# Kernel tuning notes

Measured on AMD Instinct MI355X. Metric: run time of the kernel, lower is better.

Reference implementation:

```python
import jax, jax.numpy as jnp
import numpy as np

B, NV, FD = 16, 128, 8192
T_TEMP = 0.2      # self.T
MARGIN = 1.0      # nn.TripletMarginLoss default
EPS = 1e-6        # pairwise_distance eps


def _l2norm(x):
    # torch F.normalize(dim=1): x / max(||x||, 1e-12)
    nrm = jnp.maximum(jnp.linalg.norm(x, axis=-1, keepdims=True), 1e-12)
    return x / nrm


def _ssl_parts(qb, kb, nb, num_gt):
    # qb,kb,nb: [NV, FD] flattened reid embeddings for one image
    qv = _l2norm(qb)[:num_gt]          # [g, FD]
    kv = _l2norm(kb)[:num_gt]          # [g, FD]
    nv = _l2norm(nb)                   # [NV, FD] (negatives are NOT sliced)
    g = num_gt
    S = qv @ kv.T                      # [g, g] all pairwise dots (replaces torch.dot loops)
    # similarity-matrix loss
    sm = jnp.sum((S - jnp.eye(g, dtype=S.dtype)) ** 2) / (g * g)
    # pairwise distances with torch eps convention: ||a - b + eps||_2
    # = sqrt(||a||^2 + ||b||^2 - 2 a.b + 2*eps*(sum(a)-sum(b)) + D*eps^2); ||a||=||b||=1
    sq = qv.sum(axis=1)                # [g]
    sk = kv.sum(axis=1)                # [g]
    const = FD * EPS * EPS
    d_qk = jnp.sqrt(jnp.maximum(2.0 - 2.0 * S + 2.0 * EPS * (sq[:, None] - sk[None, :]) + const, 0.0))
    d_kq = jnp.sqrt(jnp.maximum(2.0 - 2.0 * S.T + 2.0 * EPS * (sk[:, None] - sq[None, :]) + const, 0.0))
    off = 1.0 - jnp.eye(g, dtype=S.dtype)
    # triplet: anc=q_i,pos=k_i,neg=k_j  and  anc=k_i,pos=q_i,neg=q_j, j != i
    tri1 = jnp.sum(jax.nn.relu(jnp.diag(d_qk)[:, None] - d_qk + MARGIN) * off)
    tri2 = jnp.sum(jax.nn.relu(jnp.diag(d_kq)[:, None] - d_kq + MARGIN) * off)
    tri_sum = tri1 + tri2
    # cycle consistency: |q_i.k_j - k_i.q_j| = |S[i,j] - S[j,i]|
    cyc = jnp.sum(jnp.abs(S - S.T) * off) / (g * (g - 1))
    # InfoNCE: l_pos = q_i.k_i, l_neg = q @ n.T
    l_pos = jnp.diag(S)[:, None]       # [g, 1]
    l_neg = qv @ nv.T                  # [g, NV]
    logits = jnp.concatenate([l_pos, l_neg], axis=1) / T_TEMP
    ce = jnp.mean(jax.nn.logsumexp(logits, axis=1) - logits[:, 0])  # CE with labels=0
    return sm, tri_sum, cyc, ce / g


def setup_inputs() -> dict:
    key = jax.random.key(0)
    kq, kk, kn = jax.random.split(key, 3)
    q = jax.random.normal(kq, (B, NV, FD), dtype=jnp.float32)
    k = jax.random.normal(kk, (B, NV, FD), dtype=jnp.float32)
    n = jax.random.normal(kn, (B, NV, FD), dtype=jnp.float32)
    return {"q": q, "k": k, "n": n, "num_gt": NV}


def reference(q, k, n, num_gt):
    sm, tri, cyc, ce = jax.vmap(lambda a, b, c: _ssl_parts(a, b, c, num_gt))(q, k, n)
    tri_cnt = 2 * num_gt * (num_gt - 1)
    # original bug: tri_loss accumulates across batches while tri_cnt resets,
    # so each batch contributes cumsum(tri)[b] / tri_cnt
    ssl = jnp.sum(sm) + jnp.sum(jnp.cumsum(tri)) / tri_cnt + jnp.sum(cyc) + jnp.sum(ce)
    return ssl
```

## Files before the change

### kernel.cpp

```cpp
#include <hip/hip_runtime.h>
#include <cstdint>
#include <cstddef>

#define B_N   16
#define G_N   128
#define FD_N  8192
#define KCH_N 8
#define KCB   1024
#define BKB   64
#define NST   16
#define NROWS 6144

typedef unsigned short u16;
typedef u16  u16x4 __attribute__((ext_vector_type(4)));
typedef u16  u16x8 __attribute__((ext_vector_type(8)));
typedef __bf16 bf16x8 __attribute__((ext_vector_type(8)));
typedef float f32x16 __attribute__((ext_vector_type(16)));

#define QSUM_P   0
#define QSSQ_P   32768
#define KSUM_P   65536
#define KSSQ_P   98304
#define NSSQ_P   131072
#define SM_ROW   163840
#define CE_ROW   165888
#define S_OFF    167936
#define PART_OFF_F 430080
#define BF16_OFF_F 2527232

__device__ __forceinline__ u16 f2bf(float f) {
    uint32_t u = __float_as_uint(f);
    u += 0x7FFFu + ((u >> 16) & 1u);
    return (u16)(u >> 16);
}

__device__ __forceinline__ void load_lds16(const float* g, float* l) {
    __builtin_amdgcn_global_load_lds(
        (__attribute__((address_space(1))) void*)(g),
        (__attribute__((address_space(3))) void*)(l),
        16, 0, 0);
}

#define WAITV4() asm volatile("s_waitcnt vmcnt(4)" ::: "memory")
#define WAITV0() asm volatile("s_waitcnt vmcnt(0)" ::: "memory")

__global__ __launch_bounds__(256)
void k_prep(const float* __restrict__ q, const float* __restrict__ kM,
            const float* __restrict__ nM, float* __restrict__ ws)
{
    const int lane = threadIdx.x & 63;
    const int wv   = threadIdx.x >> 6;
    const int R    = blockIdx.x * 4 + wv;
    const int mat  = R >> 11;
    const int r    = R & 2047;

    const float* src = (mat == 0 ? q : (mat == 1 ? kM : nM)) + (size_t)r * FD_N;
    u16* dst = (u16*)(ws + BF16_OFF_F) + (size_t)R * FD_N;

    float ss = 0.f, qq = 0.f;
    #pragma unroll 8
    for (int j = 0; j < 32; ++j) {
        const float4 v = *(const float4*)(src + (size_t)(j*64 + lane)*4);
        ss += (v.x + v.y) + (v.z + v.w);
        qq += v.x*v.x + v.y*v.y + v.z*v.z + v.w*v.w;
        u16x4 h;
        h[0]=f2bf(v.x); h[1]=f2bf(v.y); h[2]=f2bf(v.z); h[3]=f2bf(v.w);
        *(u16x4*)(dst + (size_t)(j*64 + lane)*4) = h;
    }
    #pragma unroll
    for (int m = 32; m >= 1; m >>= 1) {
        ss += __shfl_xor(ss, m, 64);
        qq += __shfl_xor(qq, m, 64);
    }
    if (lane == 0) {
        if (mat == 0)      { ws[QSUM_P + r] = ss; ws[QSSQ_P + r] = qq; }
        else if (mat == 1) { ws[KSUM_P + r] = ss; ws[KSSQ_P + r] = qq; }
        else               { ws[NSSQ_P + r] = qq; }
    }
}

__global__ __launch_bounds__(512, 2)
void k_mm(float* __restrict__ ws)
{
    __shared__ __align__(16) u16 sA[2][G_N * BKB];
    __shared__ __align__(16) u16 sB[2][G_N * BKB];

    const int tid = threadIdx.x;
    const int blk = blockIdx.x;
    const int b    = blk >> 4;
    const int rem  = blk & 15;
    const int half = rem >> 3;
    const int kch  = rem & 7;

    const int lane  = tid & 63;
    const int wv    = tid >> 6;
    const int wm    = wv >> 2;
    const int wn    = wv & 3;
    const int khalf = lane >> 5;
    const int lrow  = lane & 31;
    const int rA0 = wm*64 + lrow;
    const int rB0 = wn*32 + lrow;

    const u16* bf = (const u16*)(ws + BF16_OFF_F);
    const u16* Abase = bf + (size_t)(b*G_N) * FD_N + kch*KCB;
    const u16* Bbase = bf + (size_t)(((half ? 2 : 1)*2048) + b*G_N) * FD_N + kch*KCB;

    const int srow = wv*16 + (lane >> 3);
    const size_t gsw = (size_t)srow * FD_N + (size_t)(((lane & 7) ^ (srow & 7)) << 3);
    const int l0 = wv * 1024;
    const int l1 = l0 + 512;

#define STAGE(ST, T) do {                                                     \
        const size_t tof_ = gsw + (size_t)((T) * BKB);                        \
        load_lds16((const float*)(Abase + tof_),            (float*)(&sA[ST][l0])); \
        load_lds16((const float*)(Bbase + tof_),            (float*)(&sB[ST][l0])); \
        load_lds16((const float*)(Abase + tof_ + 8*FD_N),   (float*)(&sA[ST][l1])); \
        load_lds16((const float*)(Bbase + tof_ + 8*FD_N),   (float*)(&sB[ST][l1])); \
    } while (0)

#define FRAG(SP, R, KC)                                                       \
    __builtin_bit_cast(bf16x8, *(const u16x8*)((SP) + (R)*BKB +               \
        ((((KC)*2 + khalf) ^ ((R)&7)) << 3)))

#define COMPUTE(ST) do {                                                      \
        const u16* dA_ = &sA[ST][0];                                          \
        const u16* dB_ = &sB[ST][0];                                          \
        __builtin_amdgcn_s_setprio(1);                                        \
        _Pragma("unroll")                                                     \
        for (int kc = 0; kc < 4; ++kc) {                                      \
            bf16x8 a0_ = FRAG(dA_, rA0,      kc);                             \
            bf16x8 a1_ = FRAG(dA_, rA0 + 32, kc);                             \
            bf16x8 b0_ = FRAG(dB_, rB0,      kc);                             \
            acc[0] = __builtin_amdgcn_mfma_f32_32x32x16_bf16(a0_, b0_, acc[0], 0,0,0); \
            acc[1] = __builtin_amdgcn_mfma_f32_32x32x16_bf16(a1_, b0_, acc[1], 0,0,0); \
        }                                                                     \
        __builtin_amdgcn_s_setprio(0);                                        \
    } while (0)

    f32x16 acc[2];
    #pragma unroll
    for (int mb = 0; mb < 2; ++mb)
      #pragma unroll
      for (int e = 0; e < 16; ++e) acc[mb][e] = 0.f;

    STAGE(0, 0);
    STAGE(1, 1);

    for (int t = 0; t < NST - 2; t += 2) {
        WAITV4();
        __builtin_amdgcn_s_barrier();
        COMPUTE(0);
        __builtin_amdgcn_s_barrier();
        STAGE(0, t + 2);

        WAITV4();
        __builtin_amdgcn_s_barrier();
        COMPUTE(1);
        __builtin_amdgcn_s_barrier();
        STAGE(1, t + 3);
    }
    WAITV4();
    __builtin_amdgcn_s_barrier();
    COMPUTE(0);
    __builtin_amdgcn_s_barrier();
    WAITV0();
    __builtin_amdgcn_s_barrier();
    COMPUTE(1);

    u16* part = (u16*)(ws + PART_OFF_F) + ((size_t)blk << 14);
    #pragma unroll
    for (int mb = 0; mb < 2; ++mb) {
        const int col = wn*32 + lrow;
        const int rbase = wm*64 + mb*32 + 4*khalf;
        #pragma unroll
        for (int reg = 0; reg < 16; ++reg) {
            const int row = rbase + (reg & 3) + 8*(reg >> 2);
            part[row*G_N + col] = f2bf(acc[mb][reg]);
        }
    }
#undef STAGE
#undef FRAG
#undef COMPUTE
}

__global__ __launch_bounds__(256)
void k_red2(float* __restrict__ ws, float* __restrict__ out)
{
    const int blk  = blockIdx.x;
    const int b    = blk >> 4;
    const int half = (blk >> 3) & 1;
    const int rg   = blk & 7;
    const int t    = threadIdx.x;
    const int lr   = t >> 4;
    const int i    = rg*16 + lr;
    const int c8   = t & 15;
    __shared__ float nrm[128];
    __shared__ float invq_s[16];

    if (blk == 0 && t == 0) out[0] = 0.f;

    if (t < 128) {
        const float ss = ws[(half ? NSSQ_P : KSSQ_P) + b*G_N + t];
        nrm[t] = 1.f / fmaxf(sqrtf(ss), 1e-12f);
    } else if (t < 144) {
        const float ss = ws[QSSQ_P + b*G_N + rg*16 + (t - 128)];
        invq_s[t-128] = 1.f / fmaxf(sqrtf(ss), 1e-12f);
    }
    __syncthreads();

    const u16* part = (const u16*)(ws + PART_OFF_F);
    float s[8] = {0,0,0,0,0,0,0,0};
    #pragma unroll
    for (int kc2 = 0; kc2 < KCH_N; ++kc2) {
        const size_t idx = ((size_t)(b*16 + half*8 + kc2) << 14) + i*G_N + c8*8;
        u16x8 h = *(const u16x8*)(part + idx);
        #pragma unroll
        for (int e = 0; e < 8; ++e)
            s[e] += __uint_as_float(((uint32_t)h[e]) << 16);
    }
    const float iq = invq_s[lr];
    if (half == 0) {
        float smacc = 0.f;
        float S8[8];
        #pragma unroll
        for (int e = 0; e < 8; ++e) {
            int j = c8*8 + e;
            S8[e] = s[e] * iq * nrm[j];
            float d = S8[e] - (j == i ? 1.f : 0.f);
            smacc += d*d;
        }
        float* Sp = ws + S_OFF + (size_t)b*16384 + i*G_N + c8*8;
        float4 w0 = {S8[0],S8[1],S8[2],S8[3]};
        float4 w1 = {S8[4],S8[5],S8[6],S8[7]};
        *(float4*)Sp = w0; *(float4*)(Sp+4) = w1;
        #pragma unroll
        for (int m = 8; m >= 1; m >>= 1) smacc += __shfl_xor(smacc, m, 64);
        if (c8 == 0) ws[SM_ROW + b*G_N + i] = smacc;
    } else {
        float eacc = 0.f;
        #pragma unroll
        for (int e = 0; e < 8; ++e)
            eacc += __expf(5.f * s[e] * iq * nrm[c8*8+e]);
        #pragma unroll
        for (int m = 8; m >= 1; m >>= 1) eacc += __shfl_xor(eacc, m, 64);
        if (c8 == 0) ws[CE_ROW + b*G_N + i] = eacc;
    }
}

__global__ __launch_bounds__(256)
void k_epi(float* __restrict__ ws, float* __restrict__ out)
{
    const int blk = blockIdx.x;
    const int b   = blk >> 3;
    const int i0  = (blk & 7) * 16;
    const int t   = threadIdx.x;
    __shared__ float sqv[128], skv[128], ddq[128], ddk[128];
    __shared__ float rbuf[4];
    const float c0 = (float)FD_N * 1e-6f * 1e-6f;

    const float* S = ws + S_OFF + (size_t)b * 16384;
    if (t < 128) {
        const float qs = ws[QSUM_P + b*G_N + t];
        const float qq = ws[QSSQ_P + b*G_N + t];
        const float ks = ws[KSUM_P + b*G_N + t];
        const float kq = ws[KSSQ_P + b*G_N + t];
        float iq = 1.f/fmaxf(sqrtf(qq),1e-12f);
        float ik = 1.f/fmaxf(sqrtf(kq),1e-12f);
        float sq = qs*iq, sk = ks*ik;
        sqv[t]=sq; skv[t]=sk;
        float Stt = S[t*G_N + t];
        ddq[t] = sqrtf(fmaxf(2.f - 2.f*Stt + 2e-6f*(sq-sk) + c0, 0.f));
        ddk[t] = sqrtf(fmaxf(2.f - 2.f*Stt + 2e-6f*(sk-sq) + c0, 0.f));
    }
    __syncthreads();

    float tri=0.f, cyc=0.f, ce=0.f, sm=0.f;
    #pragma unroll
    for (int p = 0; p < 8; ++p) {
        int idx = p*256 + t;
        int i = i0 + (idx >> 7), j = idx & 127;
        if (i != j) {
            float S_ij = S[i*G_N + j];
            float dqk = sqrtf(fmaxf(2.f - 2.f*S_ij + 2e-6f*(sqv[i]-skv[j]) + c0, 0.f));
            tri += fmaxf(ddq[i] - dqk + 1.f, 0.f);
            float dkq = sqrtf(fmaxf(2.f - 2.f*S_ij + 2e-6f*(skv[j]-sqv[i]) + c0, 0.f));
            tri += fmaxf(ddk[j] - dkq + 1.f, 0.f);
            cyc += fabsf(S_ij - S[j*G_N + i]);
        }
    }
    if (t < 16) {
        int r = i0 + t;
        float lp = 5.f * S[r*G_N + r];
        ce = __logf(ws[CE_ROW + b*G_N + r] + __expf(lp)) - lp;
        sm = ws[SM_ROW + b*G_N + r];
    }
    float contrib = sm * (1.f/16384.f) + cyc * (1.f/16256.f) + ce * (1.f/16384.f)
                  + (float)(B_N - b) * tri * (1.f/32512.f);
    #pragma unroll
    for (int m = 32; m >= 1; m >>= 1) contrib += __shfl_xor(contrib, m, 64);
    if ((t & 63) == 0) rbuf[t >> 6] = contrib;
    __syncthreads();
    if (t == 0) atomicAdd(out, rbuf[0] + rbuf[1] + rbuf[2] + rbuf[3]);
}

extern "C" void kernel_launch(void* const* d_in, const int* in_sizes, int n_in,
                              void* d_out, int out_size, void* d_ws, size_t ws_size,
                              hipStream_t stream)
{
    const float* q  = (const float*)d_in[0];
    const float* kM = (const float*)d_in[1];
    const float* nM = (const float*)d_in[2];
    float* ws  = (float*)d_ws;
    float* out = (float*)d_out;

    k_prep<<<NROWS/4, 256, 0, stream>>>(q, kM, nM, ws);
    k_mm<<<256, 512, 0, stream>>>(ws);
    k_red2<<<256, 256, 0, stream>>>(ws, out);
    k_epi<<<128, 256, 0, stream>>>(ws, out);
}
```

Measured before the change: 252.9 us.

## Fuse partial-sum reduction and epilogue into one per-batch kernel; split prep rows

The two tail kernels (partial reduction and epilogue) are merged into a single kernel with one 1024-thread block per batch element. That block holds the full 128x128 similarity matrix in LDS instead of writing it to and re-reading it from global memory, and it saves one launch. The prep kernel now splits each row across two waves, with all loads issued up front and 16-byte bf16 stores, which doubles the number of waves in flight. The output zeroing moves into the prep kernel. The tradeoff is that the fused tail runs only 16 blocks, which may underuse the GPU compared with the previous 256+128 blocks.

```diff
diff --git a/kernel.cpp b/kernel.cpp
--- a/kernel.cpp
+++ b/kernel.cpp
@@ -22,9 +22,6 @@
 #define KSUM_P   65536
 #define KSSQ_P   98304
 #define NSSQ_P   131072
-#define SM_ROW   163840
-#define CE_ROW   165888
-#define S_OFF    167936
 #define PART_OFF_F 430080
 #define BF16_OFF_F 2527232
 
@@ -46,26 +43,41 @@
 
 __global__ __launch_bounds__(256)
 void k_prep(const float* __restrict__ q, const float* __restrict__ kM,
-            const float* __restrict__ nM, float* __restrict__ ws)
+            const float* __restrict__ nM, float* __restrict__ ws,
+            float* __restrict__ out)
 {
+    if (blockIdx.x == 0 && threadIdx.x == 0) out[0] = 0.f;
+
     const int lane = threadIdx.x & 63;
     const int wv   = threadIdx.x >> 6;
-    const int R    = blockIdx.x * 4 + wv;
+    const int W    = blockIdx.x * 4 + wv;
+    const int R    = W >> 1;
+    const int h    = W & 1;
     const int mat  = R >> 11;
     const int r    = R & 2047;
 
-    const float* src = (mat == 0 ? q : (mat == 1 ? kM : nM)) + (size_t)r * FD_N;
-    u16* dst = (u16*)(ws + BF16_OFF_F) + (size_t)R * FD_N;
-
+    const float* src = (mat == 0 ? q : (mat == 1 ? kM : nM))
+                       + (size_t)r * FD_N + h * 4096;
+    u16* dst = (u16*)(ws + BF16_OFF_F) + (size_t)R * FD_N + h * 4096;
+
+    float4 v[16];
+    #pragma unroll
+    for (int j = 0; j < 8; ++j) {
+        const float* p = src + (size_t)j*512 + (size_t)lane*8;
+        v[2*j]   = *(const float4*)(p);
+        v[2*j+1] = *(const float4*)(p + 4);
+    }
     float ss = 0.f, qq = 0.f;
-    #pragma unroll 8
-    for (int j = 0; j < 32; ++j) {
-        const float4 v = *(const float4*)(src + (size_t)(j*64 + lane)*4);
-        ss += (v.x + v.y) + (v.z + v.w);
-        qq += v.x*v.x + v.y*v.y + v.z*v.z + v.w*v.w;
-        u16x4 h;
-        h[0]=f2bf(v.x); h[1]=f2bf(v.y); h[2]=f2bf(v.z); h[3]=f2bf(v.w);
-        *(u16x4*)(dst + (size_t)(j*64 + lane)*4) = h;
+    #pragma unroll
+    for (int j = 0; j < 8; ++j) {
+        const float4 lo = v[2*j], hi = v[2*j+1];
+        ss += (lo.x + lo.y) + (lo.z + lo.w) + (hi.x + hi.y) + (hi.z + hi.w);
+        qq += lo.x*lo.x + lo.y*lo.y + lo.z*lo.z + lo.w*lo.w
+            + hi.x*hi.x + hi.y*hi.y + hi.z*hi.z + hi.w*hi.w;
+        u16x8 hh;
+        hh[0]=f2bf(lo.x); hh[1]=f2bf(lo.y); hh[2]=f2bf(lo.z); hh[3]=f2bf(lo.w);
+        hh[4]=f2bf(hi.x); hh[5]=f2bf(hi.y); hh[6]=f2bf(hi.z); hh[7]=f2bf(hi.w);
+        *(u16x8*)(dst + (size_t)j*512 + (size_t)lane*8) = hh;
     }
     #pragma unroll
     for (int m = 32; m >= 1; m >>= 1) {
@@ -73,9 +85,10 @@
         qq += __shfl_xor(qq, m, 64);
     }
     if (lane == 0) {
-        if (mat == 0)      { ws[QSUM_P + r] = ss; ws[QSSQ_P + r] = qq; }
-        else if (mat == 1) { ws[KSUM_P + r] = ss; ws[KSSQ_P + r] = qq; }
-        else               { ws[NSSQ_P + r] = qq; }
+        const int o = h*2048 + r;
+        if (mat == 0)      { ws[QSUM_P + o] = ss; ws[QSSQ_P + o] = qq; }
+        else if (mat == 1) { ws[KSUM_P + o] = ss; ws[KSSQ_P + o] = qq; }
+        else               { ws[NSSQ_P + o] = qq; }
     }
 }
 
@@ -183,124 +196,130 @@
 #undef COMPUTE
 }
 
-__global__ __launch_bounds__(256)
-void k_red2(float* __restrict__ ws, float* __restrict__ out)
+__global__ __launch_bounds__(1024)
+void k_fin(float* __restrict__ ws, float* __restrict__ out)
 {
-    const int blk  = blockIdx.x;
-    const int b    = blk >> 4;
-    const int half = (blk >> 3) & 1;
-    const int rg   = blk & 7;
-    const int t    = threadIdx.x;
-    const int lr   = t >> 4;
-    const int i    = rg*16 + lr;
-    const int c8   = t & 15;
-    __shared__ float nrm[128];
-    __shared__ float invq_s[16];
-
-    if (blk == 0 && t == 0) out[0] = 0.f;
+    __shared__ float S_lds[G_N * G_N];
+    __shared__ float invq[128], nrk[128], nrn[128], sqv[128], skv[128];
+    __shared__ float ddq[128], ddk[128], smrow[128], cerow[128];
+    __shared__ float wred[16];
+
+    const int b = blockIdx.x;
+    const int t = threadIdx.x;
+    const float c0 = (float)FD_N * 1e-6f * 1e-6f;
 
     if (t < 128) {
-        const float ss = ws[(half ? NSSQ_P : KSSQ_P) + b*G_N + t];
-        nrm[t] = 1.f / fmaxf(sqrtf(ss), 1e-12f);
-    } else if (t < 144) {
-        const float ss = ws[QSSQ_P + b*G_N + rg*16 + (t - 128)];
-        invq_s[t-128] = 1.f / fmaxf(sqrtf(ss), 1e-12f);
+        const int r = b*G_N + t;
+        const float qs = ws[QSUM_P + r] + ws[QSUM_P + 2048 + r];
+        const float qq = ws[QSSQ_P + r] + ws[QSSQ_P + 2048 + r];
+        const float ks = ws[KSUM_P + r] + ws[KSUM_P + 2048 + r];
+        const float kq = ws[KSSQ_P + r] + ws[KSSQ_P + 2048 + r];
+        const float nq = ws[NSSQ_P + r] + ws[NSSQ_P + 2048 + r];
+        const float iq = 1.f / fmaxf(sqrtf(qq), 1e-12f);
+        const float ik = 1.f / fmaxf(sqrtf(kq), 1e-12f);
+        invq[t] = iq; nrk[t] = ik;
+        nrn[t]  = 1.f / fmaxf(sqrtf(nq), 1e-12f);
+        sqv[t]  = qs * iq; skv[t] = ks * ik;
     }
     __syncthreads();
 
+    const int i  = t >> 3;
+    const int c8 = t & 7;
+    const int j0 = c8 * 16;
     const u16* part = (const u16*)(ws + PART_OFF_F);
-    float s[8] = {0,0,0,0,0,0,0,0};
-    #pragma unroll
-    for (int kc2 = 0; kc2 < KCH_N; ++kc2) {
-        const size_t idx = ((size_t)(b*16 + half*8 + kc2) << 14) + i*G_N + c8*8;
-        u16x8 h = *(const u16x8*)(part + idx);
-        #pragma unroll
-        for (int e = 0; e < 8; ++e)
-            s[e] += __uint_as_float(((uint32_t)h[e]) << 16);
-    }
-    const float iq = invq_s[lr];
-    if (half == 0) {
-        float smacc = 0.f;
-        float S8[8];
-        #pragma unroll
-        for (int e = 0; e < 8; ++e) {
-            int j = c8*8 + e;
-            S8[e] = s[e] * iq * nrm[j];
-            float d = S8[e] - (j == i ? 1.f : 0.f);
-            smacc += d*d;
-        }
-        float* Sp = ws + S_OFF + (size_t)b*16384 + i*G_N + c8*8;
-        float4 w0 = {S8[0],S8[1],S8[2],S8[3]};
-        float4 w1 = {S8[4],S8[5],S8[6],S8[7]};
-        *(float4*)Sp = w0; *(float4*)(Sp+4) = w1;
-        #pragma unroll
-        for (int m = 8; m >= 1; m >>= 1) smacc += __shfl_xor(smacc, m, 64);
-        if (c8 == 0) ws[SM_ROW + b*G_N + i] = smacc;
-    } else {
-        float eacc = 0.f;
-        #pragma unroll
-        for (int e = 0; e < 8; ++e)
-            eacc += __expf(5.f * s[e] * iq * nrm[c8*8+e]);
-        #pragma unroll
-        for (int m = 8; m >= 1; m >>= 1) eacc += __shfl_xor(eacc, m, 64);
-        if (c8 == 0) ws[CE_ROW + b*G_N + i] = eacc;
-    }
-}
-
-__global__ __launch_bounds__(256)
-void k_epi(float* __restrict__ ws, float* __restrict__ out)
-{
-    const int blk = blockIdx.x;
-    const int b   = blk >> 3;
-    const int i0  = (blk & 7) * 16;
-    const int t   = threadIdx.x;
-    __shared__ float sqv[128], skv[128], ddq[128], ddk[128];
-    __shared__ float rbuf[4];
-    const float c0 = (float)FD_N * 1e-6f * 1e-6f;
-
-    const float* S = ws + S_OFF + (size_t)b * 16384;
+    const float iqv = invq[i];
+
+    {
+        float s[16];
+        #pragma unroll
+        for (int e = 0; e < 16; ++e) s[e] = 0.f;
+        #pragma unroll
+        for (int kc2 = 0; kc2 < KCH_N; ++kc2) {
+            const u16* p = part + (((size_t)(b*16 + kc2)) << 14) + i*G_N + j0;
+            const u16x8 h0 = *(const u16x8*)(p);
+            const u16x8 h1 = *(const u16x8*)(p + 8);
+            #pragma unroll
+            for (int e = 0; e < 8; ++e) {
+                s[e]   += __uint_as_float(((uint32_t)h0[e]) << 16);
+                s[e+8] += __uint_as_float(((uint32_t)h1[e]) << 16);
+            }
+        }
+        float sm = 0.f;
+        #pragma unroll
+        for (int e = 0; e < 16; ++e) {
+            const int j = j0 + e;
+            const float Sv = s[e] * iqv * nrk[j];
+            S_lds[i*G_N + j] = Sv;
+            const float d = Sv - (j == i ? 1.f : 0.f);
+            sm += d*d;
+        }
+        #pragma unroll
+        for (int m = 4; m >= 1; m >>= 1) sm += __shfl_xor(sm, m, 64);
+        if (c8 == 0) smrow[i] = sm;
+    }
+    {
+        float s[16];
+        #pragma unroll
+        for (int e = 0; e < 16; ++e) s[e] = 0.f;
+        #pragma unroll
+        for (int kc2 = 0; kc2 < KCH_N; ++kc2) {
+            const u16* p = part + (((size_t)(b*16 + 8 + kc2)) << 14) + i*G_N + j0;
+            const u16x8 h0 = *(const u16x8*)(p);
+            const u16x8 h1 = *(const u16x8*)(p + 8);
+            #pragma unroll
+            for (int e = 0; e < 8; ++e) {
+                s[e]   += __uint_as_float(((uint32_t)h0[e]) << 16);
+                s[e+8] += __uint_as_float(((uint32_t)h1[e]) << 16);
+            }
+        }
+        float ea = 0.f;
+        #pragma unroll
+        for (int e = 0; e < 16; ++e)
+            ea += __expf(5.f * s[e] * iqv * nrn[j0 + e]);
+        #pragma unroll
+        for (int m = 4; m >= 1; m >>= 1) ea += __shfl_xor(ea, m, 64);
+        if (c8 == 0) cerow[i] = ea;
+    }
+    __syncthreads();
+
     if (t < 128) {
-        const float qs = ws[QSUM_P + b*G_N + t];
-        const float qq = ws[QSSQ_P + b*G_N + t];
-        const float ks = ws[KSUM_P + b*G_N + t];
-        const float kq = ws[KSSQ_P + b*G_N + t];
-        float iq = 1.f/fmaxf(sqrtf(qq),1e-12f);
-        float ik = 1.f/fmaxf(sqrtf(kq),1e-12f);
-        float sq = qs*iq, sk = ks*ik;
-        sqv[t]=sq; skv[t]=sk;
-        float Stt = S[t*G_N + t];
-        ddq[t] = sqrtf(fmaxf(2.f - 2.f*Stt + 2e-6f*(sq-sk) + c0, 0.f));
-        ddk[t] = sqrtf(fmaxf(2.f - 2.f*Stt + 2e-6f*(sk-sq) + c0, 0.f));
+        const float Stt = S_lds[t*G_N + t];
+        ddq[t] = sqrtf(fmaxf(2.f - 2.f*Stt + 2e-6f*(sqv[t] - skv[t]) + c0, 0.f));
+        ddk[t] = sqrtf(fmaxf(2.f - 2.f*Stt + 2e-6f*(skv[t] - sqv[t]) + c0, 0.f));
     }
     __syncthreads();
 
-    float tri=0.f, cyc=0.f, ce=0.f, sm=0.f;
-    #pragma unroll
-    for (int p = 0; p < 8; ++p) {
-        int idx = p*256 + t;
-        int i = i0 + (idx >> 7), j = idx & 127;
-        if (i != j) {
-            float S_ij = S[i*G_N + j];
-            float dqk = sqrtf(fmaxf(2.f - 2.f*S_ij + 2e-6f*(sqv[i]-skv[j]) + c0, 0.f));
-            tri += fmaxf(ddq[i] - dqk + 1.f, 0.f);
-            float dkq = sqrtf(fmaxf(2.f - 2.f*S_ij + 2e-6f*(skv[j]-sqv[i]) + c0, 0.f));
-            tri += fmaxf(ddk[j] - dkq + 1.f, 0.f);
-            cyc += fabsf(S_ij - S[j*G_N + i]);
-        }
-    }
-    if (t < 16) {
-        int r = i0 + t;
-        float lp = 5.f * S[r*G_N + r];
-        ce = __logf(ws[CE_ROW + b*G_N + r] + __expf(lp)) - lp;
-        sm = ws[SM_ROW + b*G_N + r];
-    }
-    float contrib = sm * (1.f/16384.f) + cyc * (1.f/16256.f) + ce * (1.f/16384.f)
+    float tri = 0.f, cyc = 0.f, rowterm = 0.f;
+    #pragma unroll
+    for (int p2 = 0; p2 < 16; ++p2) {
+        const int idx = p2*1024 + t;
+        const int ii = idx >> 7, jj = idx & 127;
+        if (ii != jj) {
+            const float S_ij = S_lds[ii*G_N + jj];
+            const float dqk = sqrtf(fmaxf(2.f - 2.f*S_ij + 2e-6f*(sqv[ii]-skv[jj]) + c0, 0.f));
+            tri += fmaxf(ddq[ii] - dqk + 1.f, 0.f);
+            const float dkq = sqrtf(fmaxf(2.f - 2.f*S_ij + 2e-6f*(skv[jj]-sqv[ii]) + c0, 0.f));
+            tri += fmaxf(ddk[jj] - dkq + 1.f, 0.f);
+            cyc += fabsf(S_ij - S_lds[jj*G_N + ii]);
+        }
+    }
+    if (t < 128) {
+        const float lp = 5.f * S_lds[t*G_N + t];
+        const float ce = __logf(cerow[t] + __expf(lp)) - lp;
+        rowterm = smrow[t] * (1.f/16384.f) + ce * (1.f/16384.f);
+    }
+    float contrib = rowterm + cyc * (1.f/16256.f)
                   + (float)(B_N - b) * tri * (1.f/32512.f);
     #pragma unroll
     for (int m = 32; m >= 1; m >>= 1) contrib += __shfl_xor(contrib, m, 64);
-    if ((t & 63) == 0) rbuf[t >> 6] = contrib;
+    if ((t & 63) == 0) wred[t >> 6] = contrib;
     __syncthreads();
-    if (t == 0) atomicAdd(out, rbuf[0] + rbuf[1] + rbuf[2] + rbuf[3]);
+    if (t == 0) {
+        float tot = 0.f;
+        #pragma unroll
+        for (int w = 0; w < 16; ++w) tot += wred[w];
+        atomicAdd(out, tot);
+    }
 }
 
 extern "C" void kernel_launch(void* const* d_in, const int* in_sizes, int n_in,
@@ -313,8 +332,7 @@
     float* ws  = (float*)d_ws;
     float* out = (float*)d_out;
 
-    k_prep<<<NROWS/4, 256, 0, stream>>>(q, kM, nM, ws);
+    k_prep<<<NROWS*2/4, 256, 0, stream>>>(q, kM, nM, ws, out);
     k_mm<<<256, 512, 0, stream>>>(ws);
-    k_red2<<<256, 256, 0, stream>>>(ws, out);
-    k_epi<<<128, 256, 0, stream>>>(ws, out);
-}
+    k_fin<<<B_N, 1024, 0, stream>>>(ws, out);
+}
```

New measurement: 262.1 us. 3.7% more time.
